# Optimization experiments

Measured on AMD Instinct MI355X. Metric: run time of the kernel, lower is better.

The kernel has to match this reference:

```python
import jax, jax.numpy as jnp
import numpy as np

NUM_HEADS = 16
D_MODEL = 1024
D_K = D_MODEL // NUM_HEADS


def setup_inputs() -> dict:
    key = jax.random.key(0)
    ks = jax.random.split(key, 6)
    B, S = 4, 2048
    x = jax.random.normal(ks[0], (B, S, D_MODEL), dtype=jnp.float32)
    scale = 1.0 / np.sqrt(D_MODEL)
    W_q = jax.random.normal(ks[1], (D_MODEL, D_MODEL), dtype=jnp.float32) * scale
    W_k = jax.random.normal(ks[2], (D_MODEL, D_MODEL), dtype=jnp.float32) * scale
    W_v = jax.random.normal(ks[3], (D_MODEL, D_MODEL), dtype=jnp.float32) * scale
    W_o = jax.random.normal(ks[4], (D_MODEL, D_MODEL), dtype=jnp.float32) * scale
    b_o = jnp.zeros((D_MODEL,), dtype=jnp.float32)
    return {"x": x, "W_q": W_q, "W_k": W_k, "W_v": W_v, "W_o": W_o, "b_o": b_o}


def reference(x, W_q, W_k, W_v, W_o, b_o):
    B, S, D = x.shape
    H, dk = NUM_HEADS, D_K
    # torch nn.Linear computes x @ W.T
    q = (x @ W_q.T).reshape(B, S, H, dk).transpose(0, 2, 1, 3)  # [B,H,S,dk]
    k = (x @ W_k.T).reshape(B, S, H, dk).transpose(0, 2, 1, 3)
    v = (x @ W_v.T).reshape(B, S, H, dk).transpose(0, 2, 1, 3)
    scores = jnp.einsum('bhqd,bhkd->bhqk', q, k) / jnp.sqrt(jnp.float32(dk))
    causal = jnp.tril(jnp.ones((S, S), dtype=bool))  # allowed positions
    scores = jnp.where(causal[None, None], scores, -jnp.inf)
    attn = jax.nn.softmax(scores, axis=-1)
    out = jnp.einsum('bhqk,bhkd->bhqd', attn, v)
    combined = out.transpose(0, 2, 1, 3).reshape(B, S, D)
    return combined @ W_o.T + b_o
```

## Files before the change

### kernel.cpp

```cpp
#include <hip/hip_runtime.h>

typedef __attribute__((ext_vector_type(8))) short short8;
typedef __attribute__((ext_vector_type(4))) float f32x4;

#define GLOAD16(gp, lp)                                                        \
  __builtin_amdgcn_global_load_lds(                                            \
      (const __attribute__((address_space(1))) void*)(gp),                     \
      (__attribute__((address_space(3))) void*)(lp), 16, 0, 0)

__device__ __forceinline__ unsigned short f2bf(float f) {
  unsigned int u = __builtin_bit_cast(unsigned int, f);
  u += 0x7fffu + ((u >> 16) & 1u);
  return (unsigned short)(u >> 16);
}

__global__ __launch_bounds__(256) void cvt_f32_bf16(
    const float* __restrict__ src, unsigned short* __restrict__ dst, int n,
    float scale) {
  int i = (blockIdx.x * 256 + threadIdx.x) * 8;
  if (i + 8 <= n) {
    float4 a = *(const float4*)(src + i);
    float4 b = *(const float4*)(src + i + 4);
    short8 r;
    r[0] = (short)f2bf(a.x * scale); r[1] = (short)f2bf(a.y * scale);
    r[2] = (short)f2bf(a.z * scale); r[3] = (short)f2bf(a.w * scale);
    r[4] = (short)f2bf(b.x * scale); r[5] = (short)f2bf(b.y * scale);
    r[6] = (short)f2bf(b.z * scale); r[7] = (short)f2bf(b.w * scale);
    *(short8*)(dst + i) = r;
  }
}

template <int OUTF32>
__global__ __launch_bounds__(256) void gemm_nt(
    const unsigned short* __restrict__ A, const unsigned short* __restrict__ B,
    void* __restrict__ Cout, const float* __restrict__ bias, int M, int N,
    int K) {
  __shared__ __align__(16) unsigned short As[128][64];
  __shared__ __align__(16) unsigned short Bs[128][64];
  const int tid = threadIdx.x;
  const int wave = tid >> 6, lane = tid & 63;
  const int wr = wave >> 1, wc = wave & 1;
  const int l15 = lane & 15, l16 = lane >> 4;
  const int row0 = blockIdx.x * 128, col0 = blockIdx.y * 128;
  const int srow = lane >> 3;
  const int scol = (lane & 7) * 8;

  f32x4 acc[4][4] = {};

  for (int k0 = 0; k0 < K; k0 += 64) {
#pragma unroll
    for (int i = 0; i < 4; ++i) {
      const int c = i * 4 + wave;
      const unsigned short* gpa =
          A + (size_t)(row0 + c * 8 + srow) * K + k0 + scol;
      GLOAD16(gpa, &As[c * 8][0]);
      const unsigned short* gpb =
          B + (size_t)(col0 + c * 8 + srow) * K + k0 + scol;
      GLOAD16(gpb, &Bs[c * 8][0]);
    }
    __syncthreads();
#pragma unroll
    for (int kk = 0; kk < 2; ++kk) {
      short8 a[4], b[4];
#pragma unroll
      for (int m = 0; m < 4; ++m)
        a[m] = *(const short8*)&As[wr * 64 + m * 16 + l15][kk * 32 + l16 * 8];
#pragma unroll
      for (int n = 0; n < 4; ++n)
        b[n] = *(const short8*)&Bs[wc * 64 + n * 16 + l15][kk * 32 + l16 * 8];
#pragma unroll
      for (int m = 0; m < 4; ++m)
#pragma unroll
        for (int n = 0; n < 4; ++n)
          acc[m][n] =
              __builtin_amdgcn_mfma_f32_16x16x32_bf16(a[m], b[n], acc[m][n], 0, 0, 0);
    }
    __syncthreads();
  }

#pragma unroll
  for (int m = 0; m < 4; ++m) {
    const int row = row0 + wr * 64 + m * 16 + l16 * 4;
#pragma unroll
    for (int n = 0; n < 4; ++n) {
      const int col = col0 + wc * 64 + n * 16 + l15;
      float bv = 0.f;
      if (OUTF32) bv = bias[col];
#pragma unroll
      for (int r = 0; r < 4; ++r) {
        const float v = acc[m][n][r] + bv;
        if (OUTF32)
          ((float*)Cout)[(size_t)(row + r) * N + col] = v;
        else
          ((unsigned short*)Cout)[(size_t)(row + r) * N + col] = f2bf(v);
      }
    }
  }
}

__global__ __launch_bounds__(256) void attn_fwd(
    const unsigned short* __restrict__ QKV, unsigned short* __restrict__ AO) {
  const int S = 2048, LD = 3072;
  const int qt = gridDim.x - 1 - blockIdx.x;
  const int bh = blockIdx.y, b = bh >> 4, h = bh & 15;
  const int tid = threadIdx.x, wave = tid >> 6, lane = tid & 63;
  const int l15 = lane & 15, l16 = lane >> 4;
  const int q0 = qt * 64;

  __shared__ __align__(16) char KsB[2][64 * 128];
  __shared__ __align__(16) char VTB[2][64 * 128];
  __shared__ __align__(16) char PlB[4][16 * 128];

  const unsigned short* qptr =
      QKV + (size_t)(b * S + q0 + wave * 16 + l15) * LD + h * 64 + l16 * 8;
  short8 qf[2];
  qf[0] = *(const short8*)(qptr);
  qf[1] = *(const short8*)(qptr + 32);

  const int krow = lane >> 3;
  const int kcol = (((lane & 7) ^ (lane >> 3)) & 7) * 8;
  const int vp_ = tid & 31, vd0 = (tid >> 5) * 8;

  float mrow = -1e30f, lsum = 0.f;
  f32x4 accO[4] = {};
  const int nkv = qt + 1;

  {
#pragma unroll
    for (int i = 0; i < 2; ++i) {
      const int c = i * 4 + wave;
      const unsigned short* gp =
          QKV + (size_t)(b * S + c * 8 + krow) * LD + 1024 + h * 64 + kcol;
      GLOAD16(gp, KsB[0] + c * 1024);
    }
    const unsigned short* vp =
        QKV + (size_t)(b * S + 2 * vp_) * LD + 2048 + h * 64 + vd0;
    short8 va = *(const short8*)vp;
    short8 vb = *(const short8*)(vp + LD);
    uint4 vaw = __builtin_bit_cast(uint4, va);
    uint4 vbw = __builtin_bit_cast(uint4, vb);
    const unsigned int aw[4] = {vaw.x, vaw.y, vaw.z, vaw.w};
    const unsigned int bw[4] = {vbw.x, vbw.y, vbw.z, vbw.w};
#pragma unroll
    for (int w = 0; w < 4; ++w) {
      unsigned int e = __builtin_amdgcn_perm(bw[w], aw[w], 0x05040100u);
      unsigned int o = __builtin_amdgcn_perm(bw[w], aw[w], 0x07060302u);
      *(unsigned int*)(VTB[0] + (((vd0 + 2 * w) * 128 + 4 * vp_) ^ ((2 * w) << 4))) = e;
      *(unsigned int*)(VTB[0] + (((vd0 + 2 * w + 1) * 128 + 4 * vp_) ^ ((2 * w + 1) << 4))) = o;
    }
  }
  __syncthreads();

  for (int t = 0; t < nkv; ++t) {
    const int cur = t & 1, kv0 = t * 64;

    f32x4 accS[4] = {};
#pragma unroll
    for (int sub = 0; sub < 4; ++sub) {
      const int rw = sub * 16 + l15;
#pragma unroll
      for (int kk = 0; kk < 2; ++kk) {
        short8 kf = *(const short8*)(KsB[cur] + rw * 128 +
                                     ((kk * 64 + l16 * 16) ^ ((l15 & 7) << 4)));
        accS[sub] =
            __builtin_amdgcn_mfma_f32_16x16x32_bf16(kf, qf[kk], accS[sub], 0, 0, 0);
      }
    }

    short8 va, vb;
    const bool pre = (t + 1 < nkv);
    if (pre) {
      const int kvn = kv0 + 64;
#pragma unroll
      for (int i = 0; i < 2; ++i) {
        const int c = i * 4 + wave;
        const unsigned short* gp =
            QKV + (size_t)(b * S + kvn + c * 8 + krow) * LD + 1024 + h * 64 + kcol;
        GLOAD16(gp, KsB[cur ^ 1] + c * 1024);
      }
      const unsigned short* vp =
          QKV + (size_t)(b * S + kvn + 2 * vp_) * LD + 2048 + h * 64 + vd0;
      va = *(const short8*)vp;
      vb = *(const short8*)(vp + LD);
    }

    const bool nm = (kv0 + 63 > q0 + wave * 16);
    float mx = -1e30f;
    if (nm) {
      const int qabs = q0 + wave * 16 + l15;
#pragma unroll
      for (int sub = 0; sub < 4; ++sub)
#pragma unroll
        for (int r = 0; r < 4; ++r) {
          float s = accS[sub][r];
          if (kv0 + sub * 16 + l16 * 4 + r > qabs) s = -1e30f;
          accS[sub][r] = s;
          mx = fmaxf(mx, s);
        }
    } else {
#pragma unroll
      for (int sub = 0; sub < 4; ++sub)
#pragma unroll
        for (int r = 0; r < 4; ++r) mx = fmaxf(mx, accS[sub][r]);
    }
    mx = fmaxf(mx, __shfl_xor(mx, 16));
    mx = fmaxf(mx, __shfl_xor(mx, 32));

    if (__any(mx > mrow + 8.0f)) {
      const float mnew = fmaxf(mrow, mx);
      const float alpha = exp2f(mrow - mnew);
      mrow = mnew;
      lsum *= alpha;
      float al[4];
#pragma unroll
      for (int r = 0; r < 4; ++r) al[r] = __shfl(alpha, l16 * 4 + r);
#pragma unroll
      for (int sd = 0; sd < 4; ++sd)
#pragma unroll
        for (int r = 0; r < 4; ++r) accO[sd][r] *= al[r];
    }

    float rs = 0.f;
#pragma unroll
    for (int sub = 0; sub < 4; ++sub) {
      float p0 = exp2f(accS[sub][0] - mrow);
      float p1 = exp2f(accS[sub][1] - mrow);
      float p2 = exp2f(accS[sub][2] - mrow);
      float p3 = exp2f(accS[sub][3] - mrow);
      rs += (p0 + p1) + (p2 + p3);
      unsigned int pk01, pk23;
      asm("v_cvt_pk_bf16_f32 %0, %1, %2" : "=v"(pk01) : "v"(p0), "v"(p1));
      asm("v_cvt_pk_bf16_f32 %0, %1, %2" : "=v"(pk23) : "v"(p2), "v"(p3));
      uint2 pw = {pk01, pk23};
      *(uint2*)(PlB[wave] +
                ((l15 * 128 + sub * 32 + l16 * 8) ^ ((l15 & 7) << 4))) = pw;
    }
    rs += __shfl_xor(rs, 16);
    rs += __shfl_xor(rs, 32);
    lsum += rs;

    if (pre) {
      uint4 vaw = __builtin_bit_cast(uint4, va);
      uint4 vbw = __builtin_bit_cast(uint4, vb);
      const unsigned int aw[4] = {vaw.x, vaw.y, vaw.z, vaw.w};
      const unsigned int bw[4] = {vbw.x, vbw.y, vbw.z, vbw.w};
#pragma unroll
      for (int w = 0; w < 4; ++w) {
        unsigned int e = __builtin_amdgcn_perm(bw[w], aw[w], 0x05040100u);
        unsigned int o = __builtin_amdgcn_perm(bw[w], aw[w], 0x07060302u);
        *(unsigned int*)(VTB[cur ^ 1] +
                         (((vd0 + 2 * w) * 128 + 4 * vp_) ^ ((2 * w) << 4))) = e;
        *(unsigned int*)(VTB[cur ^ 1] +
                         (((vd0 + 2 * w + 1) * 128 + 4 * vp_) ^ ((2 * w + 1) << 4))) = o;
      }
    }

#pragma unroll
    for (int kk = 0; kk < 2; ++kk) {
      short8 pf = *(const short8*)(PlB[wave] + ((l15 * 128 + kk * 64 + l16 * 16) ^
                                               ((l15 & 7) << 4)));
#pragma unroll
      for (int sd = 0; sd < 4; ++sd) {
        short8 vf = *(const short8*)(VTB[cur] + (sd * 16 + l15) * 128 +
                                     ((kk * 64 + l16 * 16) ^ ((l15 & 7) << 4)));
        accO[sd] =
            __builtin_amdgcn_mfma_f32_16x16x32_bf16(pf, vf, accO[sd], 0, 0, 0);
      }
    }
    __syncthreads();
  }

  float ls[4];
#pragma unroll
  for (int r = 0; r < 4; ++r) ls[r] = __shfl(lsum, l16 * 4 + r);
#pragma unroll
  for (int sd = 0; sd < 4; ++sd)
#pragma unroll
    for (int r = 0; r < 4; ++r) {
      AO[(size_t)(b * S + q0 + wave * 16 + l16 * 4 + r) * 1024 + h * 64 +
         sd * 16 + l15] = f2bf(accO[sd][r] / ls[r]);
    }
}

extern "C" void kernel_launch(void* const* d_in, const int* in_sizes, int n_in,
                              void* d_out, int out_size, void* d_ws,
                              size_t ws_size, hipStream_t stream) {
  const float* x = (const float*)d_in[0];
  const float* Wq = (const float*)d_in[1];
  const float* Wk = (const float*)d_in[2];
  const float* Wv = (const float*)d_in[3];
  const float* Wo = (const float*)d_in[4];
  const float* bo = (const float*)d_in[5];

  char* ws = (char*)d_ws;
  unsigned short* xb = (unsigned short*)(ws);
  unsigned short* Wqkv = (unsigned short*)(ws + (size_t)(16 << 20));
  unsigned short* Wob = (unsigned short*)(ws + (size_t)(22 << 20));
  unsigned short* QKV = (unsigned short*)(ws + (size_t)(24 << 20));
  unsigned short* AO = (unsigned short*)(ws + (size_t)(72 << 20));

  const int M = 8192, D = 1024;
  const float QSCALE = 0.125f * 1.44269504088896340736f;

  cvt_f32_bf16<<<M * D / 2048, 256, 0, stream>>>(x, xb, M * D, 1.0f);
  cvt_f32_bf16<<<D * D / 2048, 256, 0, stream>>>(Wq, Wqkv, D * D, QSCALE);
  cvt_f32_bf16<<<D * D / 2048, 256, 0, stream>>>(Wk, Wqkv + D * D, D * D, 1.0f);
  cvt_f32_bf16<<<D * D / 2048, 256, 0, stream>>>(Wv, Wqkv + 2 * D * D, D * D, 1.0f);
  cvt_f32_bf16<<<D * D / 2048, 256, 0, stream>>>(Wo, Wob, D * D, 1.0f);

  dim3 g1(M / 128, 3072 / 128);
  gemm_nt<0><<<g1, 256, 0, stream>>>(xb, Wqkv, QKV, nullptr, M, 3072, D);

  dim3 g2(32, 64);
  attn_fwd<<<g2, 256, 0, stream>>>(QKV, AO);

  dim3 g3(M / 128, D / 128);
  gemm_nt<1><<<g3, 256, 0, stream>>>(AO, Wob, d_out, bo, M, D, D);
}
```

Measured before the change: 349.2 us.

## Replace GEMM with 256-row double-buffered 512-thread kernel and swizzled block order

Replaces the 128x128 single-buffered GEMM with a 256xBN tile kernel using 8 waves, double-buffered LDS staging of the next K tile during compute, and an XCD-style swizzled block index mapping. The aim is more data reuse per tile, overlap of global-to-LDS loads with MFMA work, and better L2 locality. The larger tile raises register and LDS use (128 KB at BN=256), which may lower occupancy. The trailing sync still serializes each iteration.

```diff
diff --git a/kernel.cpp b/kernel.cpp
--- a/kernel.cpp
+++ b/kernel.cpp
@@ -30,48 +30,71 @@
   }
 }
 
-template <int OUTF32>
-__global__ __launch_bounds__(256) void gemm_nt(
+template <int BN, int OUTF32>
+__global__ __launch_bounds__(512) void gemm_nt2(
     const unsigned short* __restrict__ A, const unsigned short* __restrict__ B,
     void* __restrict__ Cout, const float* __restrict__ bias, int M, int N,
-    int K) {
-  __shared__ __align__(16) unsigned short As[128][64];
-  __shared__ __align__(16) unsigned short Bs[128][64];
+    int K, int nwg_y) {
+  constexpr int NF = BN / 64;
+  constexpr int WNSZ = BN / 4;
+  __shared__ __align__(16) unsigned short As[2][256][64];
+  __shared__ __align__(16) unsigned short Bs[2][BN][64];
+
+  const int nwg = gridDim.x;
+  const int id = blockIdx.x;
+  const int sw = (id & 7) * (nwg >> 3) + (id >> 3);
+  const int bx = sw / nwg_y, by = sw % nwg_y;
+  const int row0 = bx * 256, col0 = by * BN;
+
   const int tid = threadIdx.x;
   const int wave = tid >> 6, lane = tid & 63;
-  const int wr = wave >> 1, wc = wave & 1;
+  const int wm = wave >> 2, wn = wave & 3;
   const int l15 = lane & 15, l16 = lane >> 4;
-  const int row0 = blockIdx.x * 128, col0 = blockIdx.y * 128;
-  const int srow = lane >> 3;
-  const int scol = (lane & 7) * 8;
-
-  f32x4 acc[4][4] = {};
-
-  for (int k0 = 0; k0 < K; k0 += 64) {
-#pragma unroll
-    for (int i = 0; i < 4; ++i) {
-      const int c = i * 4 + wave;
-      const unsigned short* gpa =
-          A + (size_t)(row0 + c * 8 + srow) * K + k0 + scol;
-      GLOAD16(gpa, &As[c * 8][0]);
-      const unsigned short* gpb =
-          B + (size_t)(col0 + c * 8 + srow) * K + k0 + scol;
-      GLOAD16(gpb, &Bs[c * 8][0]);
-    }
-    __syncthreads();
+  const int lrow = lane >> 3, lcol = (lane & 7) * 8;
+  const int wv8 = wave * 8;
+
+  f32x4 acc[8][NF];
+#pragma unroll
+  for (int m = 0; m < 8; ++m)
+#pragma unroll
+    for (int n = 0; n < NF; ++n) acc[m][n] = f32x4{0.f, 0.f, 0.f, 0.f};
+
+  const int nt = K >> 6;
+
+#define STAGE_TILE(buf, k0)                                                    \
+  {                                                                            \
+    _Pragma("unroll") for (int j = 0; j < 4; ++j) {                            \
+      const unsigned short* gp =                                               \
+          A + (size_t)(row0 + j * 64 + wv8 + lrow) * K + (k0) + lcol;          \
+      GLOAD16(gp, &As[buf][j * 64 + wv8][0]);                                  \
+    }                                                                          \
+    _Pragma("unroll") for (int j = 0; j < NF; ++j) {                           \
+      const unsigned short* gp =                                               \
+          B + (size_t)(col0 + j * 64 + wv8 + lrow) * K + (k0) + lcol;          \
+      GLOAD16(gp, &Bs[buf][j * 64 + wv8][0]);                                  \
+    }                                                                          \
+  }
+
+  STAGE_TILE(0, 0)
+  __syncthreads();
+
+  for (int t = 0; t < nt; ++t) {
+    const int cur = t & 1;
+    if (t + 1 < nt) STAGE_TILE(cur ^ 1, (t + 1) << 6)
+
 #pragma unroll
     for (int kk = 0; kk < 2; ++kk) {
-      short8 a[4], b[4];
-#pragma unroll
-      for (int m = 0; m < 4; ++m)
-        a[m] = *(const short8*)&As[wr * 64 + m * 16 + l15][kk * 32 + l16 * 8];
-#pragma unroll
-      for (int n = 0; n < 4; ++n)
-        b[n] = *(const short8*)&Bs[wc * 64 + n * 16 + l15][kk * 32 + l16 * 8];
-#pragma unroll
-      for (int m = 0; m < 4; ++m)
-#pragma unroll
-        for (int n = 0; n < 4; ++n)
+      short8 a[8], b[NF];
+#pragma unroll
+      for (int m = 0; m < 8; ++m)
+        a[m] = *(const short8*)&As[cur][wm * 128 + m * 16 + l15][kk * 32 + l16 * 8];
+#pragma unroll
+      for (int n = 0; n < NF; ++n)
+        b[n] = *(const short8*)&Bs[cur][wn * WNSZ + n * 16 + l15][kk * 32 + l16 * 8];
+#pragma unroll
+      for (int m = 0; m < 8; ++m)
+#pragma unroll
+        for (int n = 0; n < NF; ++n)
           acc[m][n] =
               __builtin_amdgcn_mfma_f32_16x16x32_bf16(a[m], b[n], acc[m][n], 0, 0, 0);
     }
@@ -79,11 +102,11 @@
   }
 
 #pragma unroll
-  for (int m = 0; m < 4; ++m) {
-    const int row = row0 + wr * 64 + m * 16 + l16 * 4;
-#pragma unroll
-    for (int n = 0; n < 4; ++n) {
-      const int col = col0 + wc * 64 + n * 16 + l15;
+  for (int m = 0; m < 8; ++m) {
+    const int row = row0 + wm * 128 + m * 16 + l16 * 4;
+#pragma unroll
+    for (int n = 0; n < NF; ++n) {
+      const int col = col0 + wn * WNSZ + n * 16 + l15;
       float bv = 0.f;
       if (OUTF32) bv = bias[col];
 #pragma unroll
@@ -96,6 +119,7 @@
       }
     }
   }
+#undef STAGE_TILE
 }
 
 __global__ __launch_bounds__(256) void attn_fwd(
@@ -308,12 +332,12 @@
   cvt_f32_bf16<<<D * D / 2048, 256, 0, stream>>>(Wv, Wqkv + 2 * D * D, D * D, 1.0f);
   cvt_f32_bf16<<<D * D / 2048, 256, 0, stream>>>(Wo, Wob, D * D, 1.0f);
 
-  dim3 g1(M / 128, 3072 / 128);
-  gemm_nt<0><<<g1, 256, 0, stream>>>(xb, Wqkv, QKV, nullptr, M, 3072, D);
+  gemm_nt2<256, 0><<<(M / 256) * (3072 / 256), 512, 0, stream>>>(
+      xb, Wqkv, QKV, nullptr, M, 3072, D, 3072 / 256);
 
   dim3 g2(32, 64);
   attn_fwd<<<g2, 256, 0, stream>>>(QKV, AO);
 
-  dim3 g3(M / 128, D / 128);
-  gemm_nt<1><<<g3, 256, 0, stream>>>(AO, Wob, d_out, bo, M, D, D);
-}
+  gemm_nt2<128, 1><<<(M / 256) * (D / 128), 512, 0, stream>>>(
+      AO, Wob, d_out, bo, M, D, D, D / 128);
+}
```

Result: slower. 361.8 us (+3.6%).
